# Optimization experiments

Measured on AMD Instinct MI355X. Metric: run time of the kernel, lower is better.

Reference implementation:

```python
import jax, jax.numpy as jnp
import numpy as np

N, C, E, K = 50000, 128, 640000, 40  # nodes, feat dim, edges, classes
EPS = 1e-5


def setup_inputs() -> dict:
    key = jax.random.key(0)
    ks = jax.random.split(key, 8)
    s = 1.0 / np.sqrt(C)
    return {
        "x": jax.random.normal(ks[0], (N, C), jnp.float32),
        "edge_index": jax.random.randint(ks[1], (2, E), 0, N, dtype=jnp.int32),
        "W_conv": jax.random.normal(ks[2], (C, C), jnp.float32) * s,
        "b_conv": jnp.zeros((C,), jnp.float32),
        "gamma": jnp.ones((C,), jnp.float32),
        "beta": jnp.zeros((C,), jnp.float32),
        "W_fc": jax.random.normal(ks[3], (C, K), jnp.float32) * s,
        "b_fc": jnp.zeros((K,), jnp.float32),
    }


def reference(x, edge_index, W_conv, b_conv, gamma, beta, W_fc, b_fc):
    n = x.shape[0]
    loops = jnp.arange(n, dtype=edge_index.dtype)
    src = jnp.concatenate([edge_index[0], loops])  # add self-loops (PyG default)
    dst = jnp.concatenate([edge_index[1], loops])
    # symmetric normalization: deg^{-1/2}[src] * deg^{-1/2}[dst]
    deg = jax.ops.segment_sum(jnp.ones_like(dst, jnp.float32), dst, num_segments=n)
    dinv = jax.lax.rsqrt(jnp.maximum(deg, 1.0))  # deg >= 1 with self-loops
    norm = dinv[src] * dinv[dst]  # [E+N]
    h = x @ W_conv  # [N, C] transform before propagate (GCNConv)
    agg = jax.ops.segment_sum(h[src] * norm[:, None], dst, num_segments=n) + b_conv
    a = jax.nn.relu(agg) * x  # dropout = identity (eval mode); elementwise mul with residual
    mu = jnp.mean(a, axis=-1, keepdims=True)
    var = jnp.mean((a - mu) ** 2, axis=-1, keepdims=True)
    ln = (a - mu) * jax.lax.rsqrt(var + EPS) * gamma + beta
    return (ln + x) @ W_fc + b_fc
```

## Files before the change

### kernel.cpp

```cpp
#include <hip/hip_runtime.h>

#define C_DIM 128
#define EPS 1e-5f
#define NSCAT 1250

typedef __attribute__((ext_vector_type(8))) short short8;
typedef __attribute__((ext_vector_type(4))) float f32x4;

__device__ __forceinline__ unsigned bf16rn(float f) {
    unsigned u = __float_as_uint(f);
    return (u + 0x7fffu + ((u >> 16) & 1u)) >> 16;
}
__device__ __forceinline__ unsigned pack_bf16(float lo, float hi) {
    return bf16rn(lo) | (bf16rn(hi) << 16);
}
__device__ __forceinline__ float blo(unsigned u) { return __uint_as_float(u << 16); }
__device__ __forceinline__ float bhi(unsigned u) { return __uint_as_float(u & 0xffff0000u); }

__global__ void prep0(const float* __restrict__ W, const float* __restrict__ Wfc,
                      unsigned short* __restrict__ WhT, unsigned short* __restrict__ WlT,
                      unsigned short* __restrict__ WT,
                      int* __restrict__ cntA, int* __restrict__ cntB, int n) {
    int gid = blockIdx.x * blockDim.x + threadIdx.x;
    int stride = gridDim.x * blockDim.x;
    for (int t = gid; t < 128 * 128; t += stride) {
        int c = t >> 7, k = t & 127;
        float v = W[k * 128 + c];
        unsigned hi = bf16rn(v);
        float fh = __uint_as_float(hi << 16);
        WhT[c * 128 + k] = (unsigned short)hi;
        WlT[c * 128 + k] = (unsigned short)bf16rn(v - fh);
    }
    for (int t = gid; t < 48 * 128; t += stride) {
        int nc = t >> 7, k = t & 127;
        WT[nc * 128 + k] = (unsigned short)((nc < 40) ? bf16rn(Wfc[k * 40 + nc]) : 0u);
    }
    for (int t = gid; t < n; t += stride) {
        cntA[t] = 0;
        cntB[t] = 0;
    }
}

__global__ __launch_bounds__(256, 4) void fat(const float* __restrict__ x,
                                              const unsigned short* __restrict__ WhT,
                                              const unsigned short* __restrict__ WlT,
                                              unsigned short* __restrict__ hbs,
                                              const int* __restrict__ esrc,
                                              const int* __restrict__ edst,
                                              int* __restrict__ cntA,
                                              int* __restrict__ cntB,
                                              unsigned short* __restrict__ bsrcu,
                                              int n, int e) {
    int b = blockIdx.x;
    int t = threadIdx.x;

    if (b < NSCAT) {
        int half = NSCAT * 256;
        int i = b * 256 + t;
        int j = i + half;
        if (i < e) {
            int d0 = edst[i], s0 = esrc[i];
            int p0 = atomicAdd(&cntA[d0], 1);
            if (p0 < 64) bsrcu[(long)d0 * 64 + p0] = (unsigned short)s0;
        }
        if (j < e) {
            int d1 = edst[j], s1 = esrc[j];
            int p1 = atomicAdd(&cntB[d1], 1);
            if (p1 < 64) bsrcu[(long)d1 * 64 + 63 - p1] = (unsigned short)s1;
        }
    } else {
        int r0 = (b - NSCAT) * 128;
        int wid = t >> 6, lane = t & 63;
        int mrow = lane & 15, quad = lane >> 4;
        int rb = r0 + wid * 32;

        f32x4 acc[2][8];
#pragma unroll
        for (int m = 0; m < 2; m++)
#pragma unroll
            for (int nn = 0; nn < 8; nn++) acc[m][nn] = (f32x4){0.f, 0.f, 0.f, 0.f};

#pragma unroll
        for (int ks = 0; ks < 4; ks++) {
            short8 Ah[2], Al[2];
#pragma unroll
            for (int m = 0; m < 2; m++) {
                int r = rb + m * 16 + mrow;
                if (r >= n) r = n - 1;
                const float* xp = &x[(long)r * C_DIM + ks * 32 + quad * 8];
                float4 va = *(const float4*)xp;
                float4 vb = *(const float4*)(xp + 4);
                float xv[8] = {va.x, va.y, va.z, va.w, vb.x, vb.y, vb.z, vb.w};
#pragma unroll
                for (int e8 = 0; e8 < 8; e8++) {
                    unsigned hi = bf16rn(xv[e8]);
                    Ah[m][e8] = (short)hi;
                    Al[m][e8] = (short)bf16rn(xv[e8] - __uint_as_float(hi << 16));
                }
            }
#pragma unroll
            for (int nn = 0; nn < 8; nn++) {
                int wof = (nn * 16 + mrow) * 128 + ks * 32 + quad * 8;
                short8 Bh = *(const short8*)&WhT[wof];
                short8 Bl = *(const short8*)&WlT[wof];
#pragma unroll
                for (int m = 0; m < 2; m++) {
                    acc[m][nn] = __builtin_amdgcn_mfma_f32_16x16x32_bf16(Ah[m], Bh, acc[m][nn], 0, 0, 0);
                    acc[m][nn] = __builtin_amdgcn_mfma_f32_16x16x32_bf16(Al[m], Bh, acc[m][nn], 0, 0, 0);
                    acc[m][nn] = __builtin_amdgcn_mfma_f32_16x16x32_bf16(Ah[m], Bl, acc[m][nn], 0, 0, 0);
                }
            }
        }
#pragma unroll
        for (int m = 0; m < 2; m++)
#pragma unroll
            for (int nn = 0; nn < 8; nn++) {
                int c = nn * 16 + mrow;
#pragma unroll
                for (int reg = 0; reg < 4; reg++) {
                    int r = rb + m * 16 + quad * 4 + reg;
                    if (r < n) hbs[(long)r * 128 + c] = (unsigned short)bf16rn(acc[m][nn][reg]);
                }
            }
    }
}

__global__ __launch_bounds__(256) void aggregate(const unsigned* __restrict__ hb,
                                                 const float* __restrict__ x,
                                                 const int* __restrict__ cntA,
                                                 const int* __restrict__ cntB,
                                                 const unsigned short* __restrict__ bsrcu,
                                                 const float* __restrict__ bconv,
                                                 const float* __restrict__ gamma,
                                                 const float* __restrict__ beta,
                                                 unsigned* __restrict__ zb, int n) {
    int wid = (blockIdx.x * blockDim.x + threadIdx.x) >> 6;
    if (wid >= n) return;
    int lane = threadIdx.x & 63;
    int sub = lane & 15, grp = lane >> 4;
    int i = wid;

    int dA = cntA[i], dB = cntB[i];
    float di = rsqrtf((float)(dA + dB) + 1.0f);
    if (dA > 64) dA = 64;
    if (dB > 64 - dA) dB = 64 - dA;
    int tot = dA + dB;
    int shift = 64 - tot;

    int sraw = (int)bsrcu[(long)i * 64 + lane];
    bool valid = (lane < dA) | (lane >= 64 - dB);
    int s_all = valid ? sraw : 0;
    float w_all = valid ? rsqrtf((float)(cntA[s_all] + cntB[s_all]) + 1.0f) * di : 0.f;

    uint4 us = *(const uint4*)(hb + (long)i * 64 + sub * 4);
    float wself = (grp == 0) ? di * di : 0.f;
    float acc[8];
    acc[0] = wself * blo(us.x); acc[1] = wself * bhi(us.x);
    acc[2] = wself * blo(us.y); acc[3] = wself * bhi(us.y);
    acc[4] = wself * blo(us.z); acc[5] = wself * bhi(us.z);
    acc[6] = wself * blo(us.w); acc[7] = wself * bhi(us.w);

    int nIt = (tot + 7) >> 3;
    for (int it = 0; it < nIt; ++it) {
        int t0 = grp + it * 8;
        int t1 = t0 + 4;
        int sl0 = ((t0 < dA) ? t0 : t0 + shift) & 63;
        int sl1 = ((t1 < dA) ? t1 : t1 + shift) & 63;
        int s0 = __shfl(s_all, sl0);
        float w0 = __shfl(w_all, sl0);
        int s1 = __shfl(s_all, sl1);
        float w1 = __shfl(w_all, sl1);
        if (t0 >= tot) { w0 = 0.f; s0 = i; }
        if (t1 >= tot) { w1 = 0.f; s1 = i; }
        uint4 u0 = *(const uint4*)(hb + (long)s0 * 64 + sub * 4);
        uint4 u1 = *(const uint4*)(hb + (long)s1 * 64 + sub * 4);
        acc[0] += w0 * blo(u0.x); acc[1] += w0 * bhi(u0.x);
        acc[2] += w0 * blo(u0.y); acc[3] += w0 * bhi(u0.y);
        acc[4] += w0 * blo(u0.z); acc[5] += w0 * bhi(u0.z);
        acc[6] += w0 * blo(u0.w); acc[7] += w0 * bhi(u0.w);
        acc[0] += w1 * blo(u1.x); acc[1] += w1 * bhi(u1.x);
        acc[2] += w1 * blo(u1.y); acc[3] += w1 * bhi(u1.y);
        acc[4] += w1 * blo(u1.z); acc[5] += w1 * bhi(u1.z);
        acc[6] += w1 * blo(u1.w); acc[7] += w1 * bhi(u1.w);
    }

#pragma unroll
    for (int j = 0; j < 8; j++) {
        acc[j] += __shfl_xor(acc[j], 16);
        acc[j] += __shfl_xor(acc[j], 32);
    }

    float4 bca = *(const float4*)&bconv[sub * 8];
    float4 bcb = *(const float4*)&bconv[sub * 8 + 4];
    float4 xa  = *(const float4*)&x[(long)i * C_DIM + sub * 8];
    float4 xb  = *(const float4*)&x[(long)i * C_DIM + sub * 8 + 4];
    float a[8], xv[8];
    xv[0] = xa.x; xv[1] = xa.y; xv[2] = xa.z; xv[3] = xa.w;
    xv[4] = xb.x; xv[5] = xb.y; xv[6] = xb.z; xv[7] = xb.w;
    float bc[8] = {bca.x, bca.y, bca.z, bca.w, bcb.x, bcb.y, bcb.z, bcb.w};
#pragma unroll
    for (int j = 0; j < 8; j++) a[j] = fmaxf(acc[j] + bc[j], 0.f) * xv[j];

    float s = a[0] + a[1] + a[2] + a[3] + a[4] + a[5] + a[6] + a[7];
#pragma unroll
    for (int off = 1; off < 16; off <<= 1) s += __shfl_xor(s, off);
    float mu = s * (1.0f / 128.0f);
    float d[8], v = 0.f;
#pragma unroll
    for (int j = 0; j < 8; j++) { d[j] = a[j] - mu; v += d[j] * d[j]; }
#pragma unroll
    for (int off = 1; off < 16; off <<= 1) v += __shfl_xor(v, off);
    float inv = rsqrtf(v * (1.0f / 128.0f) + EPS);

    if (grp == 0) {
        float4 ga = *(const float4*)&gamma[sub * 8];
        float4 gb = *(const float4*)&gamma[sub * 8 + 4];
        float4 ba = *(const float4*)&beta[sub * 8];
        float4 bb = *(const float4*)&beta[sub * 8 + 4];
        float g[8] = {ga.x, ga.y, ga.z, ga.w, gb.x, gb.y, gb.z, gb.w};
        float be[8] = {ba.x, ba.y, ba.z, ba.w, bb.x, bb.y, bb.z, bb.w};
        float o[8];
#pragma unroll
        for (int j = 0; j < 8; j++) o[j] = d[j] * inv * g[j] + be[j] + xv[j];
        uint4 p;
        p.x = pack_bf16(o[0], o[1]);
        p.y = pack_bf16(o[2], o[3]);
        p.z = pack_bf16(o[4], o[5]);
        p.w = pack_bf16(o[6], o[7]);
        *(uint4*)(zb + (long)i * 64 + sub * 4) = p;
    }
}

__global__ __launch_bounds__(256) void gemm2(const unsigned short* __restrict__ zb,
                                             const unsigned short* __restrict__ WT,
                                             const float* __restrict__ bfc,
                                             float* __restrict__ out, int n) {
    int t = threadIdx.x;
    int w = t >> 6, lane = t & 63;
    int r0 = (blockIdx.x * 4 + w) * 64;
    if (r0 >= n) return;
    int mrow = lane & 15;
    int quad = lane >> 4;
    f32x4 acc[4][3];
#pragma unroll
    for (int m = 0; m < 4; m++)
#pragma unroll
        for (int nt = 0; nt < 3; nt++) acc[m][nt] = (f32x4){0.f, 0.f, 0.f, 0.f};
#pragma unroll
    for (int ks = 0; ks < 4; ks++) {
        short8 A[4], B[3];
#pragma unroll
        for (int m = 0; m < 4; m++) {
            int r = r0 + m * 16 + mrow;
            if (r >= n) r = n - 1;
            A[m] = *(const short8*)&zb[(long)r * 128 + ks * 32 + quad * 8];
        }
#pragma unroll
        for (int nt = 0; nt < 3; nt++)
            B[nt] = *(const short8*)&WT[(nt * 16 + mrow) * 128 + ks * 32 + quad * 8];
#pragma unroll
        for (int m = 0; m < 4; m++)
#pragma unroll
            for (int nt = 0; nt < 3; nt++)
                acc[m][nt] = __builtin_amdgcn_mfma_f32_16x16x32_bf16(A[m], B[nt], acc[m][nt], 0, 0, 0);
    }
#pragma unroll
    for (int nt = 0; nt < 3; nt++) {
        int c = nt * 16 + mrow;
        if (c < 40) {
            float bias = bfc[c];
#pragma unroll
            for (int m = 0; m < 4; m++) {
#pragma unroll
                for (int reg = 0; reg < 4; reg++) {
                    int r = r0 + m * 16 + quad * 4 + reg;
                    if (r < n) out[(long)r * 40 + c] = acc[m][nt][reg] + bias;
                }
            }
        }
    }
}

extern "C" void kernel_launch(void* const* d_in, const int* in_sizes, int n_in,
                              void* d_out, int out_size, void* d_ws, size_t ws_size,
                              hipStream_t stream) {
    const float* x     = (const float*)d_in[0];
    const int*   ei    = (const int*)d_in[1];
    const float* Wc    = (const float*)d_in[2];
    const float* bc    = (const float*)d_in[3];
    const float* gamma = (const float*)d_in[4];
    const float* beta  = (const float*)d_in[5];
    const float* Wfc   = (const float*)d_in[6];
    const float* bfc   = (const float*)d_in[7];
    float* out = (float*)d_out;

    int N = in_sizes[0] / C_DIM;
    int E = in_sizes[1] / 2;
    const int* esrc = ei;
    const int* edst = ei + E;

    char* p = (char*)d_ws;
    auto carve = [&](size_t bytes) {
        void* q = (void*)p;
        p += (bytes + 255) & ~(size_t)255;
        return q;
    };
    unsigned* hb        = (unsigned*)carve((size_t)N * 64 * 4);
    unsigned* zb        = (unsigned*)carve((size_t)N * 64 * 4);
    unsigned short* WT  = (unsigned short*)carve(48 * 128 * 2);
    unsigned short* WhT = (unsigned short*)carve(128 * 128 * 2);
    unsigned short* WlT = (unsigned short*)carve(128 * 128 * 2);
    int* cntA           = (int*)carve((size_t)N * 4);
    int* cntB           = (int*)carve((size_t)N * 4);
    unsigned short* bsrcu = (unsigned short*)carve((size_t)N * 64 * 2);

    prep0<<<64, 256, 0, stream>>>(Wc, Wfc, WhT, WlT, WT, cntA, cntB, N);

    int g1 = (N + 127) / 128;
    fat<<<NSCAT + g1, 256, 0, stream>>>(x, WhT, WlT, (unsigned short*)hb, esrc, edst,
                                        cntA, cntB, bsrcu, N, E);

    aggregate<<<((size_t)N * 64 + 255) / 256, 256, 0, stream>>>(
        hb, x, cntA, cntB, bsrcu, bc, gamma, beta, zb, N);

    gemm2<<<(N / 64 + 4) / 4, 256, 0, stream>>>((const unsigned short*)zb, WT, bfc, out, N);
}
```

Measured before the change: 206.5 us.

## Pad edge counters, reorder fused GEMM/scatter blocks, widen aggregate gather

Each node's degree counters now sit 16 ints apart (one per 64-byte line), so the scatter atomics from different nodes no longer share a cache line. The padded arrays are zeroed with float4 stores from a larger prep grid. The fused kernel now puts the GEMM blocks first and gives each scatter thread four edges, using two cntA and two cntB slots. The aggregate kernel loads its self row and x early and unrolls the neighbour gather to four rows per iteration for more loads in flight. The cost is a counter workspace 16 times larger, more memory to zero, and sparser counter reads when computing the normalisation.

```diff
diff --git a/kernel.cpp b/kernel.cpp
--- a/kernel.cpp
+++ b/kernel.cpp
@@ -2,7 +2,7 @@
 
 #define C_DIM 128
 #define EPS 1e-5f
-#define NSCAT 1250
+#define CSTRIDE 16
 
 typedef __attribute__((ext_vector_type(8))) short short8;
 typedef __attribute__((ext_vector_type(4))) float f32x4;
@@ -20,7 +20,7 @@
 __global__ void prep0(const float* __restrict__ W, const float* __restrict__ Wfc,
                       unsigned short* __restrict__ WhT, unsigned short* __restrict__ WlT,
                       unsigned short* __restrict__ WT,
-                      int* __restrict__ cntA, int* __restrict__ cntB, int n) {
+                      float4* __restrict__ cz, int czn) {
     int gid = blockIdx.x * blockDim.x + threadIdx.x;
     int stride = gridDim.x * blockDim.x;
     for (int t = gid; t < 128 * 128; t += stride) {
@@ -35,10 +35,8 @@
         int nc = t >> 7, k = t & 127;
         WT[nc * 128 + k] = (unsigned short)((nc < 40) ? bf16rn(Wfc[k * 40 + nc]) : 0u);
     }
-    for (int t = gid; t < n; t += stride) {
-        cntA[t] = 0;
-        cntB[t] = 0;
-    }
+    float4 z = make_float4(0.f, 0.f, 0.f, 0.f);
+    for (int t = gid; t < czn; t += stride) cz[t] = z;
 }
 
 __global__ __launch_bounds__(256, 4) void fat(const float* __restrict__ x,
@@ -50,26 +48,12 @@
                                               int* __restrict__ cntA,
                                               int* __restrict__ cntB,
                                               unsigned short* __restrict__ bsrcu,
-                                              int n, int e) {
+                                              int n, int e, int g1) {
     int b = blockIdx.x;
     int t = threadIdx.x;
 
-    if (b < NSCAT) {
-        int half = NSCAT * 256;
-        int i = b * 256 + t;
-        int j = i + half;
-        if (i < e) {
-            int d0 = edst[i], s0 = esrc[i];
-            int p0 = atomicAdd(&cntA[d0], 1);
-            if (p0 < 64) bsrcu[(long)d0 * 64 + p0] = (unsigned short)s0;
-        }
-        if (j < e) {
-            int d1 = edst[j], s1 = esrc[j];
-            int p1 = atomicAdd(&cntB[d1], 1);
-            if (p1 < 64) bsrcu[(long)d1 * 64 + 63 - p1] = (unsigned short)s1;
-        }
-    } else {
-        int r0 = (b - NSCAT) * 128;
+    if (b < g1) {
+        int r0 = b * 128;
         int wid = t >> 6, lane = t & 63;
         int mrow = lane & 15, quad = lane >> 4;
         int rb = r0 + wid * 32;
@@ -122,6 +106,24 @@
                     if (r < n) hbs[(long)r * 128 + c] = (unsigned short)bf16rn(acc[m][nn][reg]);
                 }
             }
+    } else {
+        int sb = b - g1;
+        int q = (e + 3) >> 2;
+        int i0 = sb * 256 + t;
+        int i1 = i0 + q, i2 = i0 + 2 * q, i3 = i0 + 3 * q;
+        bool v0 = i0 < e, v1 = i1 < e, v2 = i2 < e, v3 = i3 < e;
+        int d0 = v0 ? edst[i0] : 0, s0 = v0 ? esrc[i0] : 0;
+        int d1 = v1 ? edst[i1] : 0, s1 = v1 ? esrc[i1] : 0;
+        int d2 = v2 ? edst[i2] : 0, s2 = v2 ? esrc[i2] : 0;
+        int d3 = v3 ? edst[i3] : 0, s3 = v3 ? esrc[i3] : 0;
+        int p0 = v0 ? atomicAdd(&cntA[(long)d0 * CSTRIDE], 1) : 64;
+        int p1 = v1 ? atomicAdd(&cntA[(long)d1 * CSTRIDE], 1) : 64;
+        int p2 = v2 ? atomicAdd(&cntB[(long)d2 * CSTRIDE], 1) : 64;
+        int p3 = v3 ? atomicAdd(&cntB[(long)d3 * CSTRIDE], 1) : 64;
+        if (p0 < 64) bsrcu[(long)d0 * 64 + p0] = (unsigned short)s0;
+        if (p1 < 64) bsrcu[(long)d1 * 64 + p1] = (unsigned short)s1;
+        if (p2 < 64) bsrcu[(long)d2 * 64 + 63 - p2] = (unsigned short)s2;
+        if (p3 < 64) bsrcu[(long)d3 * 64 + 63 - p3] = (unsigned short)s3;
     }
 }
 
@@ -140,7 +142,11 @@
     int sub = lane & 15, grp = lane >> 4;
     int i = wid;
 
-    int dA = cntA[i], dB = cntB[i];
+    uint4 us = *(const uint4*)(hb + (long)i * 64 + sub * 4);
+    float4 xa = *(const float4*)&x[(long)i * C_DIM + sub * 8];
+    float4 xb = *(const float4*)&x[(long)i * C_DIM + sub * 8 + 4];
+
+    int dA = cntA[(long)i * CSTRIDE], dB = cntB[(long)i * CSTRIDE];
     float di = rsqrtf((float)(dA + dB) + 1.0f);
     if (dA > 64) dA = 64;
     if (dB > 64 - dA) dB = 64 - dA;
@@ -150,9 +156,10 @@
     int sraw = (int)bsrcu[(long)i * 64 + lane];
     bool valid = (lane < dA) | (lane >= 64 - dB);
     int s_all = valid ? sraw : 0;
-    float w_all = valid ? rsqrtf((float)(cntA[s_all] + cntB[s_all]) + 1.0f) * di : 0.f;
-
-    uint4 us = *(const uint4*)(hb + (long)i * 64 + sub * 4);
+    float w_all = 0.f;
+    if (valid)
+        w_all = rsqrtf((float)(cntA[(long)s_all * CSTRIDE] + cntB[(long)s_all * CSTRIDE]) + 1.0f) * di;
+
     float wself = (grp == 0) ? di * di : 0.f;
     float acc[8];
     acc[0] = wself * blo(us.x); acc[1] = wself * bhi(us.x);
@@ -160,28 +167,32 @@
     acc[4] = wself * blo(us.z); acc[5] = wself * bhi(us.z);
     acc[6] = wself * blo(us.w); acc[7] = wself * bhi(us.w);
 
-    int nIt = (tot + 7) >> 3;
+    int nIt = (tot + 15) >> 4;
     for (int it = 0; it < nIt; ++it) {
-        int t0 = grp + it * 8;
-        int t1 = t0 + 4;
-        int sl0 = ((t0 < dA) ? t0 : t0 + shift) & 63;
-        int sl1 = ((t1 < dA) ? t1 : t1 + shift) & 63;
-        int s0 = __shfl(s_all, sl0);
-        float w0 = __shfl(w_all, sl0);
-        int s1 = __shfl(s_all, sl1);
-        float w1 = __shfl(w_all, sl1);
-        if (t0 >= tot) { w0 = 0.f; s0 = i; }
-        if (t1 >= tot) { w1 = 0.f; s1 = i; }
-        uint4 u0 = *(const uint4*)(hb + (long)s0 * 64 + sub * 4);
-        uint4 u1 = *(const uint4*)(hb + (long)s1 * 64 + sub * 4);
-        acc[0] += w0 * blo(u0.x); acc[1] += w0 * bhi(u0.x);
-        acc[2] += w0 * blo(u0.y); acc[3] += w0 * bhi(u0.y);
-        acc[4] += w0 * blo(u0.z); acc[5] += w0 * bhi(u0.z);
-        acc[6] += w0 * blo(u0.w); acc[7] += w0 * bhi(u0.w);
-        acc[0] += w1 * blo(u1.x); acc[1] += w1 * bhi(u1.x);
-        acc[2] += w1 * blo(u1.y); acc[3] += w1 * bhi(u1.y);
-        acc[4] += w1 * blo(u1.z); acc[5] += w1 * bhi(u1.z);
-        acc[6] += w1 * blo(u1.w); acc[7] += w1 * bhi(u1.w);
+        int tb = grp + it * 16;
+        int ss[4];
+        float ww[4];
+#pragma unroll
+        for (int qq = 0; qq < 4; qq++) {
+            int tq = tb + qq * 4;
+            int slq = ((tq < dA) ? tq : tq + shift) & 63;
+            int sq = __shfl(s_all, slq);
+            float wq = __shfl(w_all, slq);
+            if (tq >= tot) { wq = 0.f; sq = i; }
+            ss[qq] = sq;
+            ww[qq] = wq;
+        }
+        uint4 u[4];
+#pragma unroll
+        for (int qq = 0; qq < 4; qq++) u[qq] = *(const uint4*)(hb + (long)ss[qq] * 64 + sub * 4);
+#pragma unroll
+        for (int qq = 0; qq < 4; qq++) {
+            float w = ww[qq];
+            acc[0] += w * blo(u[qq].x); acc[1] += w * bhi(u[qq].x);
+            acc[2] += w * blo(u[qq].y); acc[3] += w * bhi(u[qq].y);
+            acc[4] += w * blo(u[qq].z); acc[5] += w * bhi(u[qq].z);
+            acc[6] += w * blo(u[qq].w); acc[7] += w * bhi(u[qq].w);
+        }
     }
 
 #pragma unroll
@@ -192,8 +203,6 @@
 
     float4 bca = *(const float4*)&bconv[sub * 8];
     float4 bcb = *(const float4*)&bconv[sub * 8 + 4];
-    float4 xa  = *(const float4*)&x[(long)i * C_DIM + sub * 8];
-    float4 xb  = *(const float4*)&x[(long)i * C_DIM + sub * 8 + 4];
     float a[8], xv[8];
     xv[0] = xa.x; xv[1] = xa.y; xv[2] = xa.z; xv[3] = xa.w;
     xv[4] = xb.x; xv[5] = xb.y; xv[6] = xb.z; xv[7] = xb.w;
@@ -310,15 +319,17 @@
     unsigned short* WT  = (unsigned short*)carve(48 * 128 * 2);
     unsigned short* WhT = (unsigned short*)carve(128 * 128 * 2);
     unsigned short* WlT = (unsigned short*)carve(128 * 128 * 2);
-    int* cntA           = (int*)carve((size_t)N * 4);
-    int* cntB           = (int*)carve((size_t)N * 4);
+    int* cntA           = (int*)carve((size_t)N * CSTRIDE * 4);
+    int* cntB           = (int*)carve((size_t)N * CSTRIDE * 4);
     unsigned short* bsrcu = (unsigned short*)carve((size_t)N * 64 * 2);
 
-    prep0<<<64, 256, 0, stream>>>(Wc, Wfc, WhT, WlT, WT, cntA, cntB, N);
+    int czn = (N * CSTRIDE * 2) / 4;
+    prep0<<<256, 256, 0, stream>>>(Wc, Wfc, WhT, WlT, WT, (float4*)cntA, czn);
 
     int g1 = (N + 127) / 128;
-    fat<<<NSCAT + g1, 256, 0, stream>>>(x, WhT, WlT, (unsigned short*)hb, esrc, edst,
-                                        cntA, cntB, bsrcu, N, E);
+    int nscat = (((E + 3) >> 2) + 255) / 256;
+    fat<<<g1 + nscat, 256, 0, stream>>>(x, WhT, WlT, (unsigned short*)hb, esrc, edst,
+                                        cntA, cntB, bsrcu, N, E, g1);
 
     aggregate<<<((size_t)N * 64 + 255) / 256, 256, 0, stream>>>(
         hb, x, cntA, cntB, bsrcu, bc, gamma, beta, zb, N);
```

Result: faster. 196.5 us (-4.8%).

## Replace atomic per-node edge buckets with binned counting sort and fused aggregate+LN+GEMM

Applied to the files above, without the earlier changes.

Replaces the per-node atomic bucketing of edges (capped at 64 neighbors) with a two-pass counting sort into bins of 64 destination nodes, using a block histogram, prefix scans and packed records. A per-bin kernel computes degrees. A fused mega kernel then scatter-accumulates neighbor features into shared memory with LDS float atomics, applies the normalization, ReLU, residual and LayerNorm, and runs the final GEMM from LDS, which removes the zb round trip and the separate gemm2 launch. The aim is to cut global atomics and scattered writes, but it adds extra launches, heavy LDS atomic traffic and larger per-block shared memory that limits occupancy.

```diff
diff --git a/kernel.cpp b/kernel.cpp
--- a/kernel.cpp
+++ b/kernel.cpp
@@ -2,10 +2,12 @@
 
 #define C_DIM 128
 #define EPS 1e-5f
-#define NSCAT 1250
+#define NBIN 784
+#define SBLK 8192
 
 typedef __attribute__((ext_vector_type(8))) short short8;
 typedef __attribute__((ext_vector_type(4))) float f32x4;
+typedef __attribute__((ext_vector_type(2))) float f32x2;
 
 __device__ __forceinline__ unsigned bf16rn(float f) {
     unsigned u = __float_as_uint(f);
@@ -17,59 +19,137 @@
 __device__ __forceinline__ float blo(unsigned u) { return __uint_as_float(u << 16); }
 __device__ __forceinline__ float bhi(unsigned u) { return __uint_as_float(u & 0xffff0000u); }
 
-__global__ void prep0(const float* __restrict__ W, const float* __restrict__ Wfc,
-                      unsigned short* __restrict__ WhT, unsigned short* __restrict__ WlT,
-                      unsigned short* __restrict__ WT,
-                      int* __restrict__ cntA, int* __restrict__ cntB, int n) {
-    int gid = blockIdx.x * blockDim.x + threadIdx.x;
-    int stride = gridDim.x * blockDim.x;
-    for (int t = gid; t < 128 * 128; t += stride) {
-        int c = t >> 7, k = t & 127;
-        float v = W[k * 128 + c];
-        unsigned hi = bf16rn(v);
-        float fh = __uint_as_float(hi << 16);
-        WhT[c * 128 + k] = (unsigned short)hi;
-        WlT[c * 128 + k] = (unsigned short)bf16rn(v - fh);
-    }
-    for (int t = gid; t < 48 * 128; t += stride) {
-        int nc = t >> 7, k = t & 127;
-        WT[nc * 128 + k] = (unsigned short)((nc < 40) ? bf16rn(Wfc[k * 40 + nc]) : 0u);
-    }
-    for (int t = gid; t < n; t += stride) {
-        cntA[t] = 0;
-        cntB[t] = 0;
-    }
-}
-
-__global__ __launch_bounds__(256, 4) void fat(const float* __restrict__ x,
-                                              const unsigned short* __restrict__ WhT,
-                                              const unsigned short* __restrict__ WlT,
-                                              unsigned short* __restrict__ hbs,
-                                              const int* __restrict__ esrc,
-                                              const int* __restrict__ edst,
-                                              int* __restrict__ cntA,
-                                              int* __restrict__ cntB,
-                                              unsigned short* __restrict__ bsrcu,
-                                              int n, int e) {
-    int b = blockIdx.x;
-    int t = threadIdx.x;
-
-    if (b < NSCAT) {
-        int half = NSCAT * 256;
-        int i = b * 256 + t;
-        int j = i + half;
-        if (i < e) {
-            int d0 = edst[i], s0 = esrc[i];
-            int p0 = atomicAdd(&cntA[d0], 1);
-            if (p0 < 64) bsrcu[(long)d0 * 64 + p0] = (unsigned short)s0;
-        }
-        if (j < e) {
-            int d1 = edst[j], s1 = esrc[j];
-            int p1 = atomicAdd(&cntB[d1], 1);
-            if (p1 < 64) bsrcu[(long)d1 * 64 + 63 - p1] = (unsigned short)s1;
-        }
+__device__ __forceinline__ void wave_scan_excl(unsigned* buf, int n, int lane,
+                                               unsigned* gb, unsigned* gc, bool dump) {
+    const int CH = (NBIN + 63) / 64;
+    unsigned v[CH];
+    unsigned s = 0;
+    int c0 = lane * CH;
+#pragma unroll
+    for (int k = 0; k < CH; k++) {
+        int idx = c0 + k;
+        v[k] = (idx < n) ? buf[idx] : 0u;
+        s += v[k];
+    }
+    unsigned inc = s;
+#pragma unroll
+    for (int off = 1; off < 64; off <<= 1) {
+        unsigned tmp = __shfl_up(inc, off);
+        if (lane >= off) inc += tmp;
+    }
+    unsigned run = inc - s;
+#pragma unroll
+    for (int k = 0; k < CH; k++) {
+        int idx = c0 + k;
+        if (idx < n) {
+            if (dump) { gb[idx] = run; gc[idx] = v[k]; }
+            buf[idx] = run;
+            run += v[k];
+        }
+    }
+}
+
+__global__ __launch_bounds__(256) void p0(const float* __restrict__ W,
+                                          const float* __restrict__ Wfc,
+                                          unsigned short* __restrict__ WhT,
+                                          unsigned short* __restrict__ WlT,
+                                          unsigned short* __restrict__ WT,
+                                          const int* __restrict__ edst,
+                                          unsigned* __restrict__ H, int e, int nsb) {
+    __shared__ unsigned lh[NBIN];
+    int b = blockIdx.x, t = threadIdx.x;
+    if (b < nsb) {
+        for (int k = t; k < NBIN; k += 256) lh[k] = 0u;
+        __syncthreads();
+        int e0 = b * SBLK;
+        int lim = e - e0; if (lim > SBLK) lim = SBLK;
+        for (int k = t; k < lim; k += 256) {
+            int d = edst[e0 + k];
+            atomicAdd(&lh[d >> 6], 1u);
+        }
+        __syncthreads();
+        for (int k = t; k < NBIN; k += 256) H[(size_t)k * nsb + b] = lh[k];
     } else {
-        int r0 = (b - NSCAT) * 128;
+        int gid = (b - nsb) * 256 + t;
+        int stride = ((int)gridDim.x - nsb) * 256;
+        for (int i = gid; i < 128 * 128; i += stride) {
+            int c = i >> 7, k = i & 127;
+            float v = W[k * 128 + c];
+            unsigned hi = bf16rn(v);
+            WhT[c * 128 + k] = (unsigned short)hi;
+            WlT[c * 128 + k] = (unsigned short)bf16rn(v - __uint_as_float(hi << 16));
+        }
+        for (int i = gid; i < 48 * 128; i += stride) {
+            int nc = i >> 7, k = i & 127;
+            WT[nc * 128 + k] = (unsigned short)((nc < 40) ? bf16rn(Wfc[k * 40 + nc]) : 0u);
+        }
+    }
+}
+
+__global__ __launch_bounds__(256, 3) void f1(const float* __restrict__ x,
+                                             const unsigned short* __restrict__ WhT,
+                                             const unsigned short* __restrict__ WlT,
+                                             unsigned short* __restrict__ hbs,
+                                             const int* __restrict__ esrc,
+                                             const int* __restrict__ edst,
+                                             const unsigned* __restrict__ H,
+                                             unsigned* __restrict__ recs,
+                                             unsigned* __restrict__ bstart,
+                                             unsigned* __restrict__ bcnt,
+                                             int n, int e, int nsb) {
+    __shared__ unsigned bufA[NBIN];
+    __shared__ unsigned bufB[NBIN];
+    __shared__ unsigned bufC[NBIN];
+    __shared__ unsigned sbuf[SBLK];
+    int b = blockIdx.x, t = threadIdx.x;
+
+    if (b < nsb) {
+        int e0 = b * SBLK;
+        int myE = e - e0; if (myE > SBLK) myE = SBLK;
+        for (int k = t; k < NBIN; k += 256) bufC[k] = 0u;
+        __syncthreads();
+        for (int k = t; k < myE; k += 256) {
+            int d = edst[e0 + k];
+            atomicAdd(&bufC[d >> 6], 1u);
+        }
+        for (int bin = t; bin < NBIN; bin += 256) {
+            const unsigned* row = H + (size_t)bin * nsb;
+            unsigned my = 0, tot = 0;
+            for (int sb = 0; sb < nsb; sb++) {
+                unsigned hv = row[sb];
+                tot += hv;
+                if (sb < b) my += hv;
+            }
+            bufA[bin] = tot;
+            bufB[bin] = my;
+        }
+        __syncthreads();
+        int wv = t >> 6, lane = t & 63;
+        if (wv == 0) wave_scan_excl(bufA, NBIN, lane, bstart, bcnt, b == 0);
+        else if (wv == 1) wave_scan_excl(bufC, NBIN, lane, 0, 0, false);
+        __syncthreads();
+        for (int bin = t; bin < NBIN; bin += 256) {
+            bufB[bin] += bufA[bin];
+            bufA[bin] = 0u;
+        }
+        __syncthreads();
+        for (int k = t; k < myE; k += 256) {
+            int d = edst[e0 + k];
+            int s = esrc[e0 + k];
+            int bin = d >> 6;
+            unsigned lr = atomicAdd(&bufA[bin], 1u);
+            sbuf[bufC[bin] + lr] =
+                ((unsigned)bin << 22) | ((unsigned)(d & 63) << 16) | (unsigned)s;
+        }
+        __syncthreads();
+        for (int j = t; j < myE; j += 256) {
+            unsigned rec = sbuf[j];
+            unsigned bin = rec >> 22;
+            unsigned gpos = bufB[bin] + (unsigned)j - bufC[bin];
+            recs[gpos] = rec;
+        }
+    } else {
+        int r0 = (b - nsb) * 128;
         int wid = t >> 6, lane = t & 63;
         int mrow = lane & 15, quad = lane >> 4;
         int rb = r0 + wid * 32;
@@ -125,144 +205,130 @@
     }
 }
 
-__global__ __launch_bounds__(256) void aggregate(const unsigned* __restrict__ hb,
-                                                 const float* __restrict__ x,
-                                                 const int* __restrict__ cntA,
-                                                 const int* __restrict__ cntB,
-                                                 const unsigned short* __restrict__ bsrcu,
-                                                 const float* __restrict__ bconv,
-                                                 const float* __restrict__ gamma,
-                                                 const float* __restrict__ beta,
-                                                 unsigned* __restrict__ zb, int n) {
-    int wid = (blockIdx.x * blockDim.x + threadIdx.x) >> 6;
-    if (wid >= n) return;
-    int lane = threadIdx.x & 63;
-    int sub = lane & 15, grp = lane >> 4;
-    int i = wid;
-
-    int dA = cntA[i], dB = cntB[i];
-    float di = rsqrtf((float)(dA + dB) + 1.0f);
-    if (dA > 64) dA = 64;
-    if (dB > 64 - dA) dB = 64 - dA;
-    int tot = dA + dB;
-    int shift = 64 - tot;
-
-    int sraw = (int)bsrcu[(long)i * 64 + lane];
-    bool valid = (lane < dA) | (lane >= 64 - dB);
-    int s_all = valid ? sraw : 0;
-    float w_all = valid ? rsqrtf((float)(cntA[s_all] + cntB[s_all]) + 1.0f) * di : 0.f;
-
-    uint4 us = *(const uint4*)(hb + (long)i * 64 + sub * 4);
-    float wself = (grp == 0) ? di * di : 0.f;
-    float acc[8];
-    acc[0] = wself * blo(us.x); acc[1] = wself * bhi(us.x);
-    acc[2] = wself * blo(us.y); acc[3] = wself * bhi(us.y);
-    acc[4] = wself * blo(us.z); acc[5] = wself * bhi(us.z);
-    acc[6] = wself * blo(us.w); acc[7] = wself * bhi(us.w);
-
-    int nIt = (tot + 7) >> 3;
-    for (int it = 0; it < nIt; ++it) {
-        int t0 = grp + it * 8;
-        int t1 = t0 + 4;
-        int sl0 = ((t0 < dA) ? t0 : t0 + shift) & 63;
-        int sl1 = ((t1 < dA) ? t1 : t1 + shift) & 63;
-        int s0 = __shfl(s_all, sl0);
-        float w0 = __shfl(w_all, sl0);
-        int s1 = __shfl(s_all, sl1);
-        float w1 = __shfl(w_all, sl1);
-        if (t0 >= tot) { w0 = 0.f; s0 = i; }
-        if (t1 >= tot) { w1 = 0.f; s1 = i; }
-        uint4 u0 = *(const uint4*)(hb + (long)s0 * 64 + sub * 4);
-        uint4 u1 = *(const uint4*)(hb + (long)s1 * 64 + sub * 4);
-        acc[0] += w0 * blo(u0.x); acc[1] += w0 * bhi(u0.x);
-        acc[2] += w0 * blo(u0.y); acc[3] += w0 * bhi(u0.y);
-        acc[4] += w0 * blo(u0.z); acc[5] += w0 * bhi(u0.z);
-        acc[6] += w0 * blo(u0.w); acc[7] += w0 * bhi(u0.w);
-        acc[0] += w1 * blo(u1.x); acc[1] += w1 * bhi(u1.x);
-        acc[2] += w1 * blo(u1.y); acc[3] += w1 * bhi(u1.y);
-        acc[4] += w1 * blo(u1.z); acc[5] += w1 * bhi(u1.z);
-        acc[6] += w1 * blo(u1.w); acc[7] += w1 * bhi(u1.w);
-    }
-
-#pragma unroll
-    for (int j = 0; j < 8; j++) {
-        acc[j] += __shfl_xor(acc[j], 16);
-        acc[j] += __shfl_xor(acc[j], 32);
-    }
-
-    float4 bca = *(const float4*)&bconv[sub * 8];
-    float4 bcb = *(const float4*)&bconv[sub * 8 + 4];
-    float4 xa  = *(const float4*)&x[(long)i * C_DIM + sub * 8];
-    float4 xb  = *(const float4*)&x[(long)i * C_DIM + sub * 8 + 4];
-    float a[8], xv[8];
-    xv[0] = xa.x; xv[1] = xa.y; xv[2] = xa.z; xv[3] = xa.w;
-    xv[4] = xb.x; xv[5] = xb.y; xv[6] = xb.z; xv[7] = xb.w;
-    float bc[8] = {bca.x, bca.y, bca.z, bca.w, bcb.x, bcb.y, bcb.z, bcb.w};
-#pragma unroll
-    for (int j = 0; j < 8; j++) a[j] = fmaxf(acc[j] + bc[j], 0.f) * xv[j];
-
-    float s = a[0] + a[1] + a[2] + a[3] + a[4] + a[5] + a[6] + a[7];
-#pragma unroll
-    for (int off = 1; off < 16; off <<= 1) s += __shfl_xor(s, off);
-    float mu = s * (1.0f / 128.0f);
-    float d[8], v = 0.f;
-#pragma unroll
-    for (int j = 0; j < 8; j++) { d[j] = a[j] - mu; v += d[j] * d[j]; }
-#pragma unroll
-    for (int off = 1; off < 16; off <<= 1) v += __shfl_xor(v, off);
-    float inv = rsqrtf(v * (1.0f / 128.0f) + EPS);
-
-    if (grp == 0) {
-        float4 ga = *(const float4*)&gamma[sub * 8];
-        float4 gb = *(const float4*)&gamma[sub * 8 + 4];
-        float4 ba = *(const float4*)&beta[sub * 8];
-        float4 bb = *(const float4*)&beta[sub * 8 + 4];
-        float g[8] = {ga.x, ga.y, ga.z, ga.w, gb.x, gb.y, gb.z, gb.w};
-        float be[8] = {ba.x, ba.y, ba.z, ba.w, bb.x, bb.y, bb.z, bb.w};
-        float o[8];
-#pragma unroll
-        for (int j = 0; j < 8; j++) o[j] = d[j] * inv * g[j] + be[j] + xv[j];
-        uint4 p;
-        p.x = pack_bf16(o[0], o[1]);
-        p.y = pack_bf16(o[2], o[3]);
-        p.z = pack_bf16(o[4], o[5]);
-        p.w = pack_bf16(o[6], o[7]);
-        *(uint4*)(zb + (long)i * 64 + sub * 4) = p;
-    }
-}
-
-__global__ __launch_bounds__(256) void gemm2(const unsigned short* __restrict__ zb,
-                                             const unsigned short* __restrict__ WT,
-                                             const float* __restrict__ bfc,
-                                             float* __restrict__ out, int n) {
-    int t = threadIdx.x;
-    int w = t >> 6, lane = t & 63;
-    int r0 = (blockIdx.x * 4 + w) * 64;
-    if (r0 >= n) return;
-    int mrow = lane & 15;
-    int quad = lane >> 4;
-    f32x4 acc[4][3];
-#pragma unroll
-    for (int m = 0; m < 4; m++)
-#pragma unroll
-        for (int nt = 0; nt < 3; nt++) acc[m][nt] = (f32x4){0.f, 0.f, 0.f, 0.f};
+__global__ __launch_bounds__(256) void a1(const unsigned* __restrict__ recs,
+                                          const unsigned* __restrict__ bstart,
+                                          const unsigned* __restrict__ bcnt,
+                                          float* __restrict__ dinvp) {
+    __shared__ unsigned dh[64];
+    int bin = blockIdx.x, t = threadIdx.x;
+    if (t < 64) dh[t] = 0u;
+    __syncthreads();
+    unsigned s0 = bstart[bin], cn = bcnt[bin];
+    for (unsigned k = t; k < cn; k += 256) {
+        unsigned rec = recs[s0 + k];
+        atomicAdd(&dh[(rec >> 16) & 63u], 1u);
+    }
+    __syncthreads();
+    if (t < 64) dinvp[bin * 64 + t] = rsqrtf((float)dh[t] + 1.0f);
+}
+
+__global__ __launch_bounds__(256, 3) void mega(const unsigned* __restrict__ hbu,
+                                               const float* __restrict__ x,
+                                               const unsigned* __restrict__ recs,
+                                               const float* __restrict__ dinvp,
+                                               const unsigned* __restrict__ bstart,
+                                               const unsigned* __restrict__ bcnt,
+                                               const unsigned short* __restrict__ WT,
+                                               const float* __restrict__ bconv,
+                                               const float* __restrict__ gamma,
+                                               const float* __restrict__ beta,
+                                               const float* __restrict__ bfc,
+                                               float* __restrict__ out, int n) {
+    __shared__ float accs[64 * 128];
+    __shared__ unsigned zl[64 * 70];
+    __shared__ float dvo[64];
+    int bin = blockIdx.x, t = threadIdx.x;
+    int wv = t >> 6, L = t & 63;
+
+    for (int k = t; k < 2048; k += 256) ((f32x4*)accs)[k] = (f32x4){0.f, 0.f, 0.f, 0.f};
+    if (t < 64) dvo[t] = dinvp[bin * 64 + t];
+    __syncthreads();
+
+    unsigned start = bstart[bin], cnt = bcnt[bin];
+    int nb = ((int)cnt + 63) >> 6;
+    for (int bb = wv; bb < nb; bb += 4) {
+        int k0g = bb << 6;
+        bool val = (unsigned)(k0g + L) < cnt;
+        unsigned rec = val ? recs[start + k0g + L] : 0u;
+        float wgt = val ? dinvp[rec & 0xFFFFu] : 0.f;
+#pragma unroll 1
+        for (int k0 = 0; k0 < 64; k0 += 8) {
+            unsigned rc[8]; float wk[8]; unsigned hv[8];
+#pragma unroll
+            for (int q = 0; q < 8; q++) {
+                rc[q] = __shfl(rec, k0 + q);
+                wk[q] = __shfl(wgt, k0 + q);
+            }
+#pragma unroll
+            for (int q = 0; q < 8; q++)
+                hv[q] = hbu[(size_t)(rc[q] & 0xFFFFu) * 64 + L];
+#pragma unroll
+            for (int q = 0; q < 8; q++) {
+                int row = (int)((rc[q] >> 16) & 63u);
+                __hip_atomic_fetch_add(&accs[row * 128 + L], wk[q] * blo(hv[q]),
+                                       __ATOMIC_RELAXED, __HIP_MEMORY_SCOPE_WORKGROUP);
+                __hip_atomic_fetch_add(&accs[row * 128 + 64 + L], wk[q] * bhi(hv[q]),
+                                       __ATOMIC_RELAXED, __HIP_MEMORY_SCOPE_WORKGROUP);
+            }
+        }
+    }
+    __syncthreads();
+
+#pragma unroll
+    for (int r16 = 0; r16 < 16; r16++) {
+        int row = wv * 16 + r16;
+        int node = bin * 64 + row;
+        bool vn = node < n;
+        float p0 = accs[row * 128 + L];
+        float p1 = accs[row * 128 + 64 + L];
+        unsigned hv = 0u;
+        f32x2 xv = (f32x2){0.f, 0.f};
+        if (vn) {
+            hv = hbu[(size_t)node * 64 + L];
+            xv = ((const f32x2*)x)[(size_t)node * 64 + L];
+        }
+        float dv = dvo[row];
+        p0 = dv * p0 + dv * dv * blo(hv);
+        p1 = dv * p1 + dv * dv * bhi(hv);
+        f32x2 bc = ((const f32x2*)bconv)[L];
+        float a0 = fmaxf(p0 + bc.x, 0.f) * xv.x;
+        float a1 = fmaxf(p1 + bc.y, 0.f) * xv.y;
+        float s = a0 + a1;
+#pragma unroll
+        for (int off = 1; off < 64; off <<= 1) s += __shfl_xor(s, off);
+        float mu = s * (1.0f / 128.0f);
+        float d0 = a0 - mu, d1 = a1 - mu;
+        float v = d0 * d0 + d1 * d1;
+#pragma unroll
+        for (int off = 1; off < 64; off <<= 1) v += __shfl_xor(v, off);
+        float inv = rsqrtf(v * (1.0f / 128.0f) + EPS);
+        f32x2 gm = ((const f32x2*)gamma)[L];
+        f32x2 bt = ((const f32x2*)beta)[L];
+        float o0 = d0 * inv * gm.x + bt.x + xv.x;
+        float o1 = d1 * inv * gm.y + bt.y + xv.y;
+        zl[row * 70 + L] = pack_bf16(o0, o1);
+    }
+    __syncthreads();
+
+    int mrow = L & 15, quad = L >> 4;
+    f32x4 a2[3];
+#pragma unroll
+    for (int nt = 0; nt < 3; nt++) a2[nt] = (f32x4){0.f, 0.f, 0.f, 0.f};
 #pragma unroll
     for (int ks = 0; ks < 4; ks++) {
-        short8 A[4], B[3];
-#pragma unroll
-        for (int m = 0; m < 4; m++) {
-            int r = r0 + m * 16 + mrow;
-            if (r >= n) r = n - 1;
-            A[m] = *(const short8*)&zb[(long)r * 128 + ks * 32 + quad * 8];
-        }
+        int zi = (wv * 16 + mrow) * 70 + ks * 16 + quad * 4;
+        union { unsigned u[4]; short8 s; } au;
+        au.u[0] = zl[zi + 0];
+        au.u[1] = zl[zi + 1];
+        au.u[2] = zl[zi + 2];
+        au.u[3] = zl[zi + 3];
+        short8 B[3];
 #pragma unroll
         for (int nt = 0; nt < 3; nt++)
             B[nt] = *(const short8*)&WT[(nt * 16 + mrow) * 128 + ks * 32 + quad * 8];
 #pragma unroll
-        for (int m = 0; m < 4; m++)
-#pragma unroll
-            for (int nt = 0; nt < 3; nt++)
-                acc[m][nt] = __builtin_amdgcn_mfma_f32_16x16x32_bf16(A[m], B[nt], acc[m][nt], 0, 0, 0);
+        for (int nt = 0; nt < 3; nt++)
+            a2[nt] = __builtin_amdgcn_mfma_f32_16x16x32_bf16(au.s, B[nt], a2[nt], 0, 0, 0);
     }
 #pragma unroll
     for (int nt = 0; nt < 3; nt++) {
@@ -270,12 +336,9 @@
         if (c < 40) {
             float bias = bfc[c];
 #pragma unroll
-            for (int m = 0; m < 4; m++) {
-#pragma unroll
-                for (int reg = 0; reg < 4; reg++) {
-                    int r = r0 + m * 16 + quad * 4 + reg;
-                    if (r < n) out[(long)r * 40 + c] = acc[m][nt][reg] + bias;
-                }
+            for (int reg = 0; reg < 4; reg++) {
+                int r = bin * 64 + wv * 16 + quad * 4 + reg;
+                if (r < n) out[(size_t)r * 40 + c] = a2[nt][reg] + bias;
             }
         }
     }
@@ -298,6 +361,7 @@
     int E = in_sizes[1] / 2;
     const int* esrc = ei;
     const int* edst = ei + E;
+    int nsb = (E + SBLK - 1) / SBLK;
 
     char* p = (char*)d_ws;
     auto carve = [&](size_t bytes) {
@@ -306,22 +370,21 @@
         return q;
     };
     unsigned* hb        = (unsigned*)carve((size_t)N * 64 * 4);
-    unsigned* zb        = (unsigned*)carve((size_t)N * 64 * 4);
     unsigned short* WT  = (unsigned short*)carve(48 * 128 * 2);
     unsigned short* WhT = (unsigned short*)carve(128 * 128 * 2);
     unsigned short* WlT = (unsigned short*)carve(128 * 128 * 2);
-    int* cntA           = (int*)carve((size_t)N * 4);
-    int* cntB           = (int*)carve((size_t)N * 4);
-    unsigned short* bsrcu = (unsigned short*)carve((size_t)N * 64 * 2);
-
-    prep0<<<64, 256, 0, stream>>>(Wc, Wfc, WhT, WlT, WT, cntA, cntB, N);
+    unsigned* H         = (unsigned*)carve((size_t)NBIN * nsb * 4);
+    unsigned* recs      = (unsigned*)carve((size_t)E * 4);
+    unsigned* bstart    = (unsigned*)carve((size_t)NBIN * 4);
+    unsigned* bcnt      = (unsigned*)carve((size_t)NBIN * 4);
+    float* dinvp        = (float*)carve((size_t)NBIN * 64 * 4);
 
     int g1 = (N + 127) / 128;
-    fat<<<NSCAT + g1, 256, 0, stream>>>(x, WhT, WlT, (unsigned short*)hb, esrc, edst,
-                                        cntA, cntB, bsrcu, N, E);
-
-    aggregate<<<((size_t)N * 64 + 255) / 256, 256, 0, stream>>>(
-        hb, x, cntA, cntB, bsrcu, bc, gamma, beta, zb, N);
-
-    gemm2<<<(N / 64 + 4) / 4, 256, 0, stream>>>((const unsigned short*)zb, WT, bfc, out, N);
-}
+
+    p0<<<nsb + 64, 256, 0, stream>>>(Wc, Wfc, WhT, WlT, WT, edst, H, E, nsb);
+    f1<<<nsb + g1, 256, 0, stream>>>(x, WhT, WlT, (unsigned short*)hb, esrc, edst, H,
+                                     recs, bstart, bcnt, N, E, nsb);
+    a1<<<NBIN, 256, 0, stream>>>(recs, bstart, bcnt, dinvp);
+    mega<<<NBIN, 256, 0, stream>>>(hb, x, recs, dinvp, bstart, bcnt, WT, bc, gamma,
+                                   beta, bfc, out, N);
+}
```

New measurement: 757.4 us. 3.67x slower.
